# Kernel optimization log

Measured on AMD Instinct MI355X. Metric: run time of the kernel, lower is better.

## Reference

```python
import jax, jax.numpy as jnp
import numpy as np

B, S, V, D, H, NL, FF, MAXD, OUTLEN, NC = 8, 1024, 64, 512, 8, 6, 2048, 64, 8, 10
HD = D // H


def _layernorm(x, g, b, eps=1e-5):
    m = jnp.mean(x, axis=-1, keepdims=True)
    v = jnp.var(x, axis=-1, keepdims=True)
    return (x - m) * jax.lax.rsqrt(v + eps) * g + b


def setup_inputs() -> dict:
    key = jax.random.key(0)
    ks = jax.random.split(key, 24)
    s = 0.02
    inp = {
        'src': jax.random.randint(ks[0], (B, S), 0, V, dtype=jnp.int32),
        'src_pad_mask': jnp.zeros((B, S), dtype=bool),
        'embed': jax.random.normal(ks[1], (V, D), jnp.float32) * s,
        'cls_token': jnp.zeros((D,), jnp.float32),
        'qkv_w': jax.random.normal(ks[2], (NL, 3 * D, D), jnp.float32) * s,
        'qkv_b': jnp.zeros((NL, 3 * D), jnp.float32),
        'out_w': jax.random.normal(ks[3], (NL, D, D), jnp.float32) * s,
        'out_b': jnp.zeros((NL, D), jnp.float32),
        'rel_emb': jax.random.normal(ks[4], (NL, 2 * MAXD + 1, H), jnp.float32) * s,
        'ln1_g': jnp.ones((NL, D), jnp.float32),
        'ln1_b': jnp.zeros((NL, D), jnp.float32),
        'w1': jax.random.normal(ks[5], (NL, FF, D), jnp.float32) * s,
        'b1': jnp.zeros((NL, FF), jnp.float32),
        'w2': jax.random.normal(ks[6], (NL, D, FF), jnp.float32) * s,
        'b2': jnp.zeros((NL, D), jnp.float32),
        'ln2_g': jnp.ones((NL, D), jnp.float32),
        'ln2_b': jnp.zeros((NL, D), jnp.float32),
        'norm_g': jnp.ones((D,), jnp.float32),
        'norm_b': jnp.zeros((D,), jnp.float32),
        'cls_w': jax.random.normal(ks[7], (OUTLEN * NC, D), jnp.float32) * s,
        'cls_b': jnp.zeros((OUTLEN * NC,), jnp.float32),
    }
    return inp


def _forward(src, src_pad_mask, embed, cls_token, qkv_w, qkv_b, out_w, out_b,
             rel_emb, ln1_g, ln1_b, w1, b1, w2, b2, ln2_g, ln2_b,
             norm_g, norm_b, cls_w, cls_b):
    b = src.shape[0]
    x = embed[src]                                         # [B,S,D]
    cls = jnp.broadcast_to(cls_token, (b, 1, D))
    x = jnp.concatenate([cls, x], axis=1)                  # [B,L,D], L=S+1
    L = x.shape[1]
    full_mask = jnp.concatenate([jnp.zeros((b, 1), bool), src_pad_mask], axis=1)

    # relative position indices, shared across layers
    rel = jnp.arange(L)[None, :] - jnp.arange(L)[:, None]  # [L,L]
    maxd = (rel_emb.shape[1] - 1) // 2
    rel = jnp.clip(rel, -maxd, maxd) + maxd
    scale = HD ** -0.5
    neg = jnp.asarray(-1e9, x.dtype)

    def layer(x, p):
        (qw, qb, ow, ob, re, g1, be1, W1, B1, W2, B2, g2, be2) = p
        qkv = jnp.einsum('bld,ed->ble', x, qw) + qb        # [B,L,3D]
        q, k, v = jnp.split(qkv, 3, axis=-1)
        q = q.reshape(b, L, H, HD)
        k = k.reshape(b, L, H, HD)
        v = v.reshape(b, L, H, HD)
        scores = jnp.einsum('bqhd,bkhd->bhqk', q, k) * scale
        bias = re[rel]                                     # [L,L,H]
        scores = scores + jnp.transpose(bias, (2, 0, 1))[None]
        scores = jnp.where(full_mask[:, None, None, :], neg, scores)
        attn = jax.nn.softmax(scores, axis=-1)
        o = jnp.einsum('bhqk,bkhd->bqhd', attn, v).reshape(b, L, D)
        o = jnp.einsum('bld,ed->ble', o, ow) + ob
        x2 = _layernorm(x + o, g1, be1)
        h = jax.nn.gelu(jnp.einsum('bld,fd->blf', x2, W1) + B1, approximate=False)
        ff = jnp.einsum('blf,df->bld', h, W2) + B2
        x3 = _layernorm(x2 + ff, g2, be2)
        return x3, None

    xs = (qkv_w, qkv_b, out_w, out_b, rel_emb, ln1_g, ln1_b,
          w1, b1, w2, b2, ln2_g, ln2_b)
    x, _ = jax.lax.scan(layer, x, xs)
    x = _layernorm(x, norm_g, norm_b)
    cls_repr = x[:, 0, :]
    logits = jnp.einsum('bd,od->bo', cls_repr, cls_w) + cls_b
    return logits.reshape(b, OUTLEN, NC)


def reference(src, src_pad_mask, embed, cls_token, qkv_w, qkv_b, out_w, out_b,
              rel_emb, ln1_g, ln1_b, w1, b1, w2, b2, ln2_g, ln2_b,
              norm_g, norm_b, cls_w, cls_b):
    return _forward(src, src_pad_mask, embed, cls_token, qkv_w, qkv_b, out_w,
                    out_b, rel_emb, ln1_g, ln1_b, w1, b1, w2, b2, ln2_g,
                    ln2_b, norm_g, norm_b, cls_w, cls_b)
```

## Files before the change

### kernel.cpp

```cpp
#include <hip/hip_runtime.h>
#include <hip/hip_bf16.h>
#include <stdint.h>

#define B 8
#define S 1024
#define L 1025
#define D 512
#define H 8
#define HD 64
#define NL 6
#define FF 2048
#define MAXD 64
#define OUTLEN 8
#define NC 10

#define MP 8320

typedef __bf16 bf16;
typedef __bf16 bf16x8 __attribute__((ext_vector_type(8)));
typedef __bf16 bf16x4 __attribute__((ext_vector_type(4)));
typedef float f32x4 __attribute__((ext_vector_type(4)));

__device__ __forceinline__ float fexp2(float x) { return __builtin_amdgcn_exp2f(x); }

#define LGKM_BARRIER() asm volatile("s_waitcnt lgkmcnt(0)\ns_barrier" ::: "memory")

__device__ __forceinline__ void gld16(const void* g, void* l) {
    __builtin_amdgcn_global_load_lds(
        (const __attribute__((address_space(1))) unsigned int*)g,
        (__attribute__((address_space(3))) unsigned int*)l,
        16, 0, 0);
}

__device__ __forceinline__ float fast_gelu(float v) {
    float x = v * 0.70710678118654752f;
    float ax = fabsf(x);
    float t = 1.f / fmaf(0.3275911f, ax, 1.f);
    float poly = t * (0.254829592f + t * (-0.284496736f + t * (1.421413741f +
                 t * (-1.453152027f + t * 1.061405429f))));
    float e = fexp2(-ax * ax * 1.4426950408889634f);
    float erfv = 1.f - poly * e;
    erfv = copysignf(erfv, x);
    return 0.5f * v * (1.f + erfv);
}

__global__ __launch_bounds__(256) void cvt_k(const float* __restrict__ in,
                                             bf16* __restrict__ out, int n4)
{
    int i = blockIdx.x * 256 + threadIdx.x;
    if (i >= n4) return;
    float4 v = reinterpret_cast<const float4*>(in)[i];
    bf16x4 o;
    o[0] = (bf16)v.x; o[1] = (bf16)v.y; o[2] = (bf16)v.z; o[3] = (bf16)v.w;
    reinterpret_cast<bf16x4*>(out)[i] = o;
}

__global__ void embed_k(const int* __restrict__ src, const float* __restrict__ emb,
                        const float* __restrict__ cls, float* __restrict__ x,
                        bf16* __restrict__ xb)
{
    long i = (long)blockIdx.x * blockDim.x + threadIdx.x;
    if (i >= (long)B * L * D) return;
    int d = (int)(i % D);
    long bl = i / D;
    int l = (int)(bl % L);
    int b = (int)(bl / L);
    float v = (l == 0) ? cls[d] : emb[(long)src[b * S + (l - 1)] * D + d];
    x[i] = v;
    xb[i] = (bf16)v;
}

template<int ACT, int OBF, int BIAS, int RT>
__global__ __launch_bounds__(256) void mgemm(const bf16* __restrict__ A,
                                             const bf16* __restrict__ W,
                                             const float* __restrict__ bias,
                                             float* __restrict__ Cf,
                                             bf16* __restrict__ Cb,
                                             int N, int K, int LDA)
{
    __shared__ bf16 Asl[2][RT * 32];
    __shared__ bf16 Bsl[2][128 * 32];
    int tid = threadIdx.x;
    int m0 = blockIdx.y * RT;
    int n0 = blockIdx.x * 128;
    int lane = tid & 63;
    int w = tid >> 6;
    int wbase = tid & ~63;
    int kb = (lane >> 4) * 8;
    int rsel = lane & 15;
    constexpr int FJ = (RT == 128) ? 4 : 2;
    constexpr int CW = (RT == 128) ? 64 : 32;
    int wr, wc;
    if constexpr (RT == 128) { wr = w >> 1; wc = w & 1; }
    else                     { wr = 0;      wc = w;     }
    f32x4 acc[4][FJ] = {};

    auto stage = [&](int buf, int k0) {
        if constexpr (RT == 128) {
#pragma unroll
            for (int r = 0; r < 2; r++) {
                int s = r * 256 + tid;
                int sb = r * 256 + wbase;
                gld16(A + (size_t)(m0 + (s >> 2)) * LDA + k0 + (s & 3) * 8, &Asl[buf][(size_t)sb * 8]);
                gld16(W + (size_t)(n0 + (s >> 2)) * LDA + k0 + (s & 3) * 8, &Bsl[buf][(size_t)sb * 8]);
            }
        } else {
            gld16(A + (size_t)(m0 + (tid >> 2)) * LDA + k0 + (tid & 3) * 8, &Asl[buf][(size_t)wbase * 8]);
#pragma unroll
            for (int r = 0; r < 2; r++) {
                int s = r * 256 + tid;
                int sb = r * 256 + wbase;
                gld16(W + (size_t)(n0 + (s >> 2)) * LDA + k0 + (s & 3) * 8, &Bsl[buf][(size_t)sb * 8]);
            }
        }
    };

    stage(0, 0);
    __syncthreads();

    for (int k0 = 0; k0 < K; k0 += 32) {
        int cur = (k0 >> 5) & 1;
        if (k0 + 32 < K) stage(cur ^ 1, k0 + 32);
        bf16x8 af[4], bfr[FJ];
#pragma unroll
        for (int fi = 0; fi < 4; fi++)
            af[fi] = *reinterpret_cast<const bf16x8*>(&Asl[cur][(wr * 64 + fi * 16 + rsel) * 32 + kb]);
#pragma unroll
        for (int fj = 0; fj < FJ; fj++)
            bfr[fj] = *reinterpret_cast<const bf16x8*>(&Bsl[cur][(wc * CW + fj * 16 + rsel) * 32 + kb]);
#pragma unroll
        for (int fi = 0; fi < 4; fi++)
#pragma unroll
            for (int fj = 0; fj < FJ; fj++)
                acc[fi][fj] = __builtin_amdgcn_mfma_f32_16x16x32_bf16(af[fi], bfr[fj], acc[fi][fj], 0, 0, 0);
        __syncthreads();
    }
    int rowb = (lane >> 4) * 4;
    int colb = lane & 15;
#pragma unroll
    for (int fi = 0; fi < 4; fi++) {
#pragma unroll
        for (int fj = 0; fj < FJ; fj++) {
            int col = n0 + wc * CW + fj * 16 + colb;
            float bsv = BIAS ? bias[col] : 0.f;
#pragma unroll
            for (int i = 0; i < 4; i++) {
                int row = m0 + wr * 64 + fi * 16 + rowb + i;
                float v = acc[fi][fj][i] + bsv;
                if (ACT) v = fast_gelu(v);
                if (OBF) Cb[(size_t)row * N + col] = (bf16)v;
                else     Cf[(size_t)row * N + col] = v;
            }
        }
    }
}

__global__ __launch_bounds__(256) void fattn_k(const bf16* __restrict__ qkv,
                                               const float* __restrict__ rel_emb_l,
                                               const unsigned char* __restrict__ pad,
                                               bf16* __restrict__ ob)
{
    constexpr int PIT = 72;
    __shared__ bf16 Vt[3][64 * PIT];
    __shared__ bf16 Psh[4][2][16 * PIT];
    __shared__ float bias2s[2 * MAXD + 1];
    __shared__ float colm[2][64];

    const int bh = blockIdx.x;
    const int qt = blockIdx.y;
    const int h = bh & 7, b = bh >> 3;
    const int q0 = qt * 128;
    const int tid = threadIdx.x;
    const int lane = tid & 63;
    const int w = tid >> 6;
    const int ln15 = lane & 15, g4 = lane >> 4;
    const int kb8 = g4 * 8;
    constexpr float LOG2E = 1.4426950408889634f;
    constexpr float C2 = 0.125f * LOG2E;

    const char* base = (const char*)qkv + (size_t)(b * L) * 3072 + (size_t)h * (HD * 2);

    for (int i = tid; i < 2 * MAXD + 1; i += 256) bias2s[i] = rel_emb_l[i * H + h] * LOG2E;
    if (tid < 64) colm[0][tid] = (tid > 0 && pad[(size_t)b * S + tid - 1]) ? -1e9f : 0.f;

    int qrow[2];
    bf16x8 qa[2][2];
#pragma unroll
    for (int qq = 0; qq < 2; qq++) {
        qrow[qq] = q0 + qq * 64 + w * 16 + ln15;
        qa[qq][0] = *(const bf16x8*)(base + (size_t)qrow[qq] * 3072 + g4 * 16);
        qa[qq][1] = *(const bf16x8*)(base + (size_t)qrow[qq] * 3072 + 64 + g4 * 16);
    }

    const int vr = tid >> 3;
    const int vd0 = (tid & 7) * 8;
    const int vsw = ((vd0 >> 3) & 7) << 3;

    {
        bf16x8 a = *(const bf16x8*)(base + (size_t)vr * 3072 + 2048 + vd0 * 2);
        bf16x8 c = *(const bf16x8*)(base + (size_t)(vr + 32) * 3072 + 2048 + vd0 * 2);
#pragma unroll
        for (int j = 0; j < 8; j++) {
            Vt[0][(vd0 + j) * PIT + (vr ^ vsw)] = a[j];
            Vt[0][(vd0 + j) * PIT + ((vr + 32) ^ vsw)] = c[j];
        }
    }
    bf16x8 kr[4][2];
#pragma unroll
    for (int fj = 0; fj < 4; fj++) {
        const char* rp = base + (size_t)(fj * 16 + ln15) * 3072 + 1024 + g4 * 16;
        kr[fj][0] = *(const bf16x8*)(rp);
        kr[fj][1] = *(const bf16x8*)(rp + 64);
    }
    LGKM_BARRIER();

    f32x4 oacc[2][4] = {};
    float m_prev[2] = {-1e30f, -1e30f};
    float l_sum[2] = {0.f, 0.f};

    int cur3 = 0;
    for (int t = 0; t < 17; t++) {
        const int k0 = t * 64;
        const int k0n = (k0 + 64 > 1024) ? 1024 : (k0 + 64);
        const int curM = t & 1;
        int nxt3 = cur3 + 1; if (nxt3 == 3) nxt3 = 0;

        bf16x8 vA = *(const bf16x8*)(base + (size_t)(k0n + vr) * 3072 + 2048 + vd0 * 2);
        bf16x8 vB = *(const bf16x8*)(base + (size_t)(k0n + vr + 32) * 3072 + 2048 + vd0 * 2);

        f32x4 sacc[2][4] = {};
#pragma unroll
        for (int qq = 0; qq < 2; qq++)
#pragma unroll
            for (int fj = 0; fj < 4; fj++) {
                sacc[qq][fj] = __builtin_amdgcn_mfma_f32_16x16x32_bf16(kr[fj][0], qa[qq][0], sacc[qq][fj], 0, 0, 0);
                sacc[qq][fj] = __builtin_amdgcn_mfma_f32_16x16x32_bf16(kr[fj][1], qa[qq][1], sacc[qq][fj], 0, 0, 0);
            }
#pragma unroll
        for (int fj = 0; fj < 4; fj++) {
            const char* rp = base + (size_t)(k0n + fj * 16 + ln15) * 3072 + 1024 + g4 * 16;
            kr[fj][0] = *(const bf16x8*)(rp);
            kr[fj][1] = *(const bf16x8*)(rp + 64);
        }

        f32x4 cm[4];
#pragma unroll
        for (int fj = 0; fj < 4; fj++)
            cm[fj] = *(const f32x4*)&colm[curM][fj * 16 + g4 * 4];

#pragma unroll
        for (int qq = 0; qq < 2; qq++) {
            float sv[4][4];
            const int relbw = k0 - q0 - qq * 64 - w * 16;
            if (relbw >= MAXD + 15 || relbw <= -MAXD - 63) {
                const float bu = bias2s[relbw > 0 ? 2 * MAXD : 0];
#pragma unroll
                for (int fj = 0; fj < 4; fj++)
#pragma unroll
                    for (int i = 0; i < 4; i++)
                        sv[fj][i] = fmaf(sacc[qq][fj][i], C2, bu + cm[fj][i]);
            } else {
                const int relb = k0 - qrow[qq];
#pragma unroll
                for (int fj = 0; fj < 4; fj++)
#pragma unroll
                    for (int i = 0; i < 4; i++) {
                        int rel = relb + fj * 16 + g4 * 4 + i;
                        rel = rel < -MAXD ? -MAXD : (rel > MAXD ? MAXD : rel);
                        sv[fj][i] = fmaf(sacc[qq][fj][i], C2, bias2s[rel + MAXD] + cm[fj][i]);
                    }
            }

            float mx = sv[0][0];
#pragma unroll
            for (int fj = 0; fj < 4; fj++)
#pragma unroll
                for (int i = 0; i < 4; i++) mx = fmaxf(mx, sv[fj][i]);
            mx = fmaxf(mx, __shfl_xor(mx, 16));
            mx = fmaxf(mx, __shfl_xor(mx, 32));
            const float mnew = fmaxf(m_prev[qq], mx);
            const float corr = fexp2(m_prev[qq] - mnew);
            float rsum = 0.f;
            float pb[4][4];
#pragma unroll
            for (int fj = 0; fj < 4; fj++)
#pragma unroll
                for (int i = 0; i < 4; i++) {
                    float p = fexp2(sv[fj][i] - mnew);
                    pb[fj][i] = p;
                    rsum += p;
                }
            rsum += __shfl_xor(rsum, 16);
            rsum += __shfl_xor(rsum, 32);
            l_sum[qq] = l_sum[qq] * corr + rsum;
            m_prev[qq] = mnew;
#pragma unroll
            for (int fd = 0; fd < 4; fd++) oacc[qq][fd] *= corr;

#pragma unroll
            for (int fj = 0; fj < 4; fj++) {
                union { bf16 hh[4]; unsigned long long u; } pk;
                pk.hh[0] = (bf16)pb[fj][0]; pk.hh[1] = (bf16)pb[fj][1];
                pk.hh[2] = (bf16)pb[fj][2]; pk.hh[3] = (bf16)pb[fj][3];
                *(unsigned long long*)&Psh[w][qq][ln15 * PIT + fj * 16 + g4 * 4] = pk.u;
            }
        }

#pragma unroll
        for (int j = 0; j < 8; j++) {
            Vt[nxt3][(vd0 + j) * PIT + (vr ^ vsw)] = vA[j];
            Vt[nxt3][(vd0 + j) * PIT + ((vr + 32) ^ vsw)] = vB[j];
        }
        if (tid < 64) {
            int gk = k0 + 64 + tid;
            int pi = (gk <= 1024) ? gk - 1 : 0;
            colm[curM ^ 1][tid] = (gk > 1024 || pad[(size_t)b * S + pi]) ? -1e9f : 0.f;
        }

        LGKM_BARRIER();

        bf16x8 pa[2][2];
#pragma unroll
        for (int qq = 0; qq < 2; qq++) {
            pa[qq][0] = *(const bf16x8*)&Psh[w][qq][ln15 * PIT + kb8];
            pa[qq][1] = *(const bf16x8*)&Psh[w][qq][ln15 * PIT + 32 + kb8];
        }
#pragma unroll
        for (int fd = 0; fd < 4; fd++) {
            const int d = fd * 16 + ln15;
            const int vx = ((d >> 3) & 7) << 3;
            bf16x8 af0 = *(const bf16x8*)&Vt[cur3][d * PIT + (kb8 ^ vx)];
            bf16x8 af1 = *(const bf16x8*)&Vt[cur3][d * PIT + ((32 + kb8) ^ vx)];
            oacc[0][fd] = __builtin_amdgcn_mfma_f32_16x16x32_bf16(af0, pa[0][0], oacc[0][fd], 0, 0, 0);
            oacc[0][fd] = __builtin_amdgcn_mfma_f32_16x16x32_bf16(af1, pa[0][1], oacc[0][fd], 0, 0, 0);
            oacc[1][fd] = __builtin_amdgcn_mfma_f32_16x16x32_bf16(af0, pa[1][0], oacc[1][fd], 0, 0, 0);
            oacc[1][fd] = __builtin_amdgcn_mfma_f32_16x16x32_bf16(af1, pa[1][1], oacc[1][fd], 0, 0, 0);
        }
        cur3 = nxt3;
    }

#pragma unroll
    for (int qq = 0; qq < 2; qq++) {
        if (qrow[qq] < L) {
            const float inv = 1.f / l_sum[qq];
            bf16* op = ob + (size_t)(b * L + qrow[qq]) * D + h * HD + g4 * 4;
#pragma unroll
            for (int fd = 0; fd < 4; fd++) {
                bf16x4 r;
#pragma unroll
                for (int i = 0; i < 4; i++) r[i] = (bf16)(oacc[qq][fd][i] * inv);
                *(bf16x4*)(op + fd * 16) = r;
            }
        }
    }
}

__global__ __launch_bounds__(256) void add_ln_k(const float* __restrict__ xin,
                                                const float* __restrict__ rin,
                                                const float* __restrict__ g,
                                                const float* __restrict__ bb,
                                                float* __restrict__ out,
                                                bf16* __restrict__ outb)
{
    int row = blockIdx.x;
    __shared__ float red[8];
    int tid = threadIdx.x;
    const float* xp = xin + (size_t)row * D;
    const float* rp = rin + (size_t)row * D;
    float v0 = xp[tid] + rp[tid];
    float v1 = xp[tid + 256] + rp[tid + 256];
    float s = v0 + v1;
    for (int off = 32; off; off >>= 1) s += __shfl_down(s, off, 64);
    int lane = tid & 63, wid = tid >> 6;
    if (lane == 0) red[wid] = s;
    __syncthreads();
    if (tid == 0) red[0] = red[0] + red[1] + red[2] + red[3];
    __syncthreads();
    float mean = red[0] * (1.f / D);
    float d0 = v0 - mean, d1 = v1 - mean;
    float sq = d0 * d0 + d1 * d1;
    for (int off = 32; off; off >>= 1) sq += __shfl_down(sq, off, 64);
    if (lane == 0) red[4 + wid] = sq;
    __syncthreads();
    if (tid == 0) red[4] = red[4] + red[5] + red[6] + red[7];
    __syncthreads();
    float rs = rsqrtf(red[4] * (1.f / D) + 1e-5f);
    float r0 = d0 * rs * g[tid] + bb[tid];
    float r1 = d1 * rs * g[tid + 256] + bb[tid + 256];
    out[(size_t)row * D + tid] = r0;
    out[(size_t)row * D + tid + 256] = r1;
    outb[(size_t)row * D + tid] = (bf16)r0;
    outb[(size_t)row * D + tid + 256] = (bf16)r1;
}

__global__ __launch_bounds__(256) void cls_k(const float* __restrict__ x,
                                             const float* __restrict__ ng,
                                             const float* __restrict__ nb,
                                             const float* __restrict__ cw,
                                             const float* __restrict__ cb,
                                             float* __restrict__ out)
{
    int b = blockIdx.x;
    __shared__ float xn[D];
    __shared__ float red[8];
    int tid = threadIdx.x;
    const float* xp = x + (size_t)(b * L) * D;
    float v0 = xp[tid], v1 = xp[tid + 256];
    float s = v0 + v1;
    for (int off = 32; off; off >>= 1) s += __shfl_down(s, off, 64);
    int lane = tid & 63, wid = tid >> 6;
    if (lane == 0) red[wid] = s;
    __syncthreads();
    if (tid == 0) red[0] = red[0] + red[1] + red[2] + red[3];
    __syncthreads();
    float mean = red[0] * (1.f / D);
    float d0 = v0 - mean, d1 = v1 - mean;
    float sq = d0 * d0 + d1 * d1;
    for (int off = 32; off; off >>= 1) sq += __shfl_down(sq, off, 64);
    if (lane == 0) red[4 + wid] = sq;
    __syncthreads();
    if (tid == 0) red[4] = red[4] + red[5] + red[6] + red[7];
    __syncthreads();
    float rs = rsqrtf(red[4] * (1.f / D) + 1e-5f);
    xn[tid] = d0 * rs * ng[tid] + nb[tid];
    xn[tid + 256] = d1 * rs * ng[tid + 256] + nb[tid + 256];
    __syncthreads();
    for (int o = tid; o < OUTLEN * NC; o += 256) {
        float acc = cb[o];
        const float* wp = cw + (size_t)o * D;
        for (int d = 0; d < D; d++) acc += xn[d] * wp[d];
        out[b * OUTLEN * NC + o] = acc;
    }
}

extern "C" void kernel_launch(void* const* d_in, const int* in_sizes, int n_in,
                              void* d_out, int out_size, void* d_ws, size_t ws_size,
                              hipStream_t stream) {
    const int* src = (const int*)d_in[0];
    const unsigned char* pad = (const unsigned char*)d_in[1];
    const float* emb = (const float*)d_in[2];
    const float* cls_token = (const float*)d_in[3];
    const float* qkv_w = (const float*)d_in[4];
    const float* qkv_b = (const float*)d_in[5];
    const float* out_w = (const float*)d_in[6];
    const float* out_b = (const float*)d_in[7];
    const float* rel_emb = (const float*)d_in[8];
    const float* ln1_g = (const float*)d_in[9];
    const float* ln1_b = (const float*)d_in[10];
    const float* w1 = (const float*)d_in[11];
    const float* b1 = (const float*)d_in[12];
    const float* w2 = (const float*)d_in[13];
    const float* b2 = (const float*)d_in[14];
    const float* ln2_g = (const float*)d_in[15];
    const float* ln2_b = (const float*)d_in[16];
    const float* norm_g = (const float*)d_in[17];
    const float* norm_b = (const float*)d_in[18];
    const float* cls_w = (const float*)d_in[19];
    const float* cls_b = (const float*)d_in[20];
    float* out = (float*)d_out;

    char* ws = (char*)d_ws;
    size_t off = 0;
    float* x   = (float*)(ws + off); off += (size_t)MP * D * 4;
    bf16*  xb  = (bf16*) (ws + off); off += (size_t)MP * D * 2;
    float* x2  = (float*)(ws + off); off += (size_t)MP * D * 4;
    bf16*  x2b = (bf16*) (ws + off); off += (size_t)MP * D * 2;
    char*  R   = ws + off;           off += (size_t)MP * 3 * D * 4;
    bf16*  qkvb = (bf16*)R;
    bf16*  hb  = (bf16*)R;
    float* p   = (float*)(R + (size_t)MP * FF * 2);
    bf16*  obf = (bf16*) (ws + off); off += (size_t)MP * D * 2;

    const size_t WQ = (size_t)NL * 3 * D * D;
    const size_t WO = (size_t)NL * D * D;
    const size_t W1E = (size_t)NL * FF * D;
    const size_t W2E = (size_t)NL * D * FF;
    const size_t WALL = WQ + WO + W1E + W2E;
    bool all_w = (off + WALL * 2) <= ws_size;

    bf16 *wq_a = nullptr, *wo_a = nullptr, *w1_a = nullptr, *w2_a = nullptr, *wbuf = nullptr;
    if (all_w) {
        wq_a = (bf16*)(ws + off);
        wo_a = wq_a + WQ;
        w1_a = wo_a + WO;
        w2_a = w1_a + W1E;
        int n4;
        n4 = (int)(WQ / 4);  cvt_k<<<dim3((n4 + 255) / 256), 256, 0, stream>>>(qkv_w, wq_a, n4);
        n4 = (int)(WO / 4);  cvt_k<<<dim3((n4 + 255) / 256), 256, 0, stream>>>(out_w, wo_a, n4);
        n4 = (int)(W1E / 4); cvt_k<<<dim3((n4 + 255) / 256), 256, 0, stream>>>(w1, w1_a, n4);
        n4 = (int)(W2E / 4); cvt_k<<<dim3((n4 + 255) / 256), 256, 0, stream>>>(w2, w2_a, n4);
    } else {
        wbuf = (bf16*)(ws + off);
    }

    const int M = B * L;
    {
        long total = (long)B * L * D;
        embed_k<<<dim3((unsigned)((total + 255) / 256)), 256, 0, stream>>>(src, emb, cls_token, x, xb);
    }
    for (int l = 0; l < NL; l++) {
        const float* qb  = qkv_b + (size_t)l * 3 * D;
        const float* obi = out_b + (size_t)l * D;
        const float* re  = rel_emb + (size_t)l * (2 * MAXD + 1) * H;
        const float* g1  = ln1_g + (size_t)l * D;
        const float* be1 = ln1_b + (size_t)l * D;
        const float* B1p = b1 + (size_t)l * FF;
        const float* B2p = b2 + (size_t)l * D;
        const float* g2  = ln2_g + (size_t)l * D;
        const float* be2 = ln2_b + (size_t)l * D;

        const bf16 *wqb, *wob, *w1b, *w2b;
        if (all_w) {
            wqb = wq_a + (size_t)l * 3 * D * D;
            wob = wo_a + (size_t)l * D * D;
            w1b = w1_a + (size_t)l * FF * D;
            w2b = w2_a + (size_t)l * D * FF;
        } else {
            bf16* wp_ = wbuf;
            wqb = wp_;            wp_ += 3 * D * D;
            wob = wp_;            wp_ += D * D;
            w1b = wp_;            wp_ += FF * D;
            w2b = wp_;
            int n4;
            n4 = 3 * D * D / 4; cvt_k<<<dim3((n4 + 255) / 256), 256, 0, stream>>>(qkv_w + (size_t)l * 3 * D * D, (bf16*)wqb, n4);
            n4 = D * D / 4;     cvt_k<<<dim3((n4 + 255) / 256), 256, 0, stream>>>(out_w + (size_t)l * D * D, (bf16*)wob, n4);
            n4 = FF * D / 4;    cvt_k<<<dim3((n4 + 255) / 256), 256, 0, stream>>>(w1 + (size_t)l * FF * D, (bf16*)w1b, n4);
            n4 = D * FF / 4;    cvt_k<<<dim3((n4 + 255) / 256), 256, 0, stream>>>(w2 + (size_t)l * D * FF, (bf16*)w2b, n4);
        }

        mgemm<0, 1, 1, 128><<<dim3(3 * D / 128, MP / 128), 256, 0, stream>>>(xb, wqb, qb, nullptr, qkvb, 3 * D, D, D);
        fattn_k<<<dim3(B * H, 9), 256, 0, stream>>>(qkvb, re, pad, obf);
        mgemm<0, 0, 1, 64><<<dim3(D / 128, MP / 64), 256, 0, stream>>>(obf, wob, obi, p, nullptr, D, D, D);
        add_ln_k<<<dim3(M), 256, 0, stream>>>(x, p, g1, be1, x2, x2b);
        mgemm<1, 1, 1, 128><<<dim3(FF / 128, MP / 128), 256, 0, stream>>>(x2b, w1b, B1p, nullptr, hb, FF, D, D);
        mgemm<0, 0, 1, 64><<<dim3(D / 128, MP / 64), 256, 0, stream>>>(hb, w2b, B2p, p, nullptr, D, FF, FF);
        add_ln_k<<<dim3(M), 256, 0, stream>>>(x2, p, g2, be2, x, xb);
    }
    cls_k<<<dim3(B), 256, 0, stream>>>(x, norm_g, norm_b, cls_w, cls_b, out);
}
```

Measured before the change: 1.475 ms.

## Split attention over key range into two partials and merge with combine kernel

Adds a split-K (flash-decoding style) partition of the attention key loop: each block processes half of the key tiles and writes a partial normalized output plus per-row max and sum, then a new combine kernel merges the two halves using log-sum-exp rescaling. This doubles the grid from 576 blocks so more of the GPU's compute units are busy, since the original grid was small relative to the device. In exchange it adds an extra kernel launch, extra global traffic for partial outputs and stats, and an additional bf16 rounding of partial results. Scratch buffers x2b and p are reused for partials and stats.

New measurement: 1.463 ms. About the same (-0.8%).

```diff
diff --git a/kernel.cpp b/kernel.cpp
--- a/kernel.cpp
+++ b/kernel.cpp
@@ -158,7 +158,9 @@
 __global__ __launch_bounds__(256) void fattn_k(const bf16* __restrict__ qkv,
                                                const float* __restrict__ rel_emb_l,
                                                const unsigned char* __restrict__ pad,
-                                               bf16* __restrict__ ob)
+                                               bf16* __restrict__ op0,
+                                               bf16* __restrict__ op1,
+                                               float2* __restrict__ mlout)
 {
     constexpr int PIT = 72;
     __shared__ bf16 Vt[3][64 * PIT];
@@ -168,6 +170,10 @@
 
     const int bh = blockIdx.x;
     const int qt = blockIdx.y;
+    const int z = blockIdx.z;
+    const int tbeg = z ? 9 : 0;
+    const int tend = z ? 17 : 9;
+    bf16* opart = z ? op1 : op0;
     const int h = bh & 7, b = bh >> 3;
     const int q0 = qt * 128;
     const int tid = threadIdx.x;
@@ -181,7 +187,11 @@
     const char* base = (const char*)qkv + (size_t)(b * L) * 3072 + (size_t)h * (HD * 2);
 
     for (int i = tid; i < 2 * MAXD + 1; i += 256) bias2s[i] = rel_emb_l[i * H + h] * LOG2E;
-    if (tid < 64) colm[0][tid] = (tid > 0 && pad[(size_t)b * S + tid - 1]) ? -1e9f : 0.f;
+    if (tid < 64) {
+        int gk0 = tbeg * 64 + tid;
+        int pi = (gk0 > 0 && gk0 <= 1024) ? gk0 - 1 : 0;
+        colm[tbeg & 1][tid] = (gk0 > 1024 || (gk0 > 0 && pad[(size_t)b * S + pi])) ? -1e9f : 0.f;
+    }
 
     int qrow[2];
     bf16x8 qa[2][2];
@@ -197,8 +207,9 @@
     const int vsw = ((vd0 >> 3) & 7) << 3;
 
     {
-        bf16x8 a = *(const bf16x8*)(base + (size_t)vr * 3072 + 2048 + vd0 * 2);
-        bf16x8 c = *(const bf16x8*)(base + (size_t)(vr + 32) * 3072 + 2048 + vd0 * 2);
+        int kv0 = tbeg * 64;
+        bf16x8 a = *(const bf16x8*)(base + (size_t)(kv0 + vr) * 3072 + 2048 + vd0 * 2);
+        bf16x8 c = *(const bf16x8*)(base + (size_t)(kv0 + vr + 32) * 3072 + 2048 + vd0 * 2);
 #pragma unroll
         for (int j = 0; j < 8; j++) {
             Vt[0][(vd0 + j) * PIT + (vr ^ vsw)] = a[j];
@@ -208,7 +219,7 @@
     bf16x8 kr[4][2];
 #pragma unroll
     for (int fj = 0; fj < 4; fj++) {
-        const char* rp = base + (size_t)(fj * 16 + ln15) * 3072 + 1024 + g4 * 16;
+        const char* rp = base + (size_t)(tbeg * 64 + fj * 16 + ln15) * 3072 + 1024 + g4 * 16;
         kr[fj][0] = *(const bf16x8*)(rp);
         kr[fj][1] = *(const bf16x8*)(rp + 64);
     }
@@ -219,7 +230,7 @@
     float l_sum[2] = {0.f, 0.f};
 
     int cur3 = 0;
-    for (int t = 0; t < 17; t++) {
+    for (int t = tbeg; t < tend; t++) {
         const int k0 = t * 64;
         const int k0n = (k0 + 64 > 1024) ? 1024 : (k0 + 64);
         const int curM = t & 1;
@@ -343,7 +354,7 @@
     for (int qq = 0; qq < 2; qq++) {
         if (qrow[qq] < L) {
             const float inv = 1.f / l_sum[qq];
-            bf16* op = ob + (size_t)(b * L + qrow[qq]) * D + h * HD + g4 * 4;
+            bf16* op = opart + (size_t)(b * L + qrow[qq]) * D + h * HD + g4 * 4;
 #pragma unroll
             for (int fd = 0; fd < 4; fd++) {
                 bf16x4 r;
@@ -351,7 +362,35 @@
                 for (int i = 0; i < 4; i++) r[i] = (bf16)(oacc[qq][fd][i] * inv);
                 *(bf16x4*)(op + fd * 16) = r;
             }
-        }
+            if (g4 == 0)
+                mlout[(size_t)(z * 64 + b * 8 + h) * 1025 + qrow[qq]] =
+                    make_float2(m_prev[qq], l_sum[qq]);
+        }
+    }
+}
+
+__global__ __launch_bounds__(256) void comb_k(const bf16* __restrict__ op0,
+                                              const bf16* __restrict__ op1,
+                                              const float2* __restrict__ ml,
+                                              bf16* __restrict__ ob)
+{
+    int row = blockIdx.x;
+    int b = row / L, q = row - b * L;
+    int tid = threadIdx.x;
+    int d = tid & 63;
+    int h0 = tid >> 6;
+#pragma unroll
+    for (int hh = 0; hh < 2; hh++) {
+        int h = h0 + hh * 4;
+        float2 a = ml[(size_t)(b * 8 + h) * 1025 + q];
+        float2 c = ml[(size_t)(64 + b * 8 + h) * 1025 + q];
+        float m = fmaxf(a.x, c.x);
+        float s1 = a.y * fexp2(a.x - m);
+        float s2 = c.y * fexp2(c.x - m);
+        float inv = 1.f / (s1 + s2);
+        size_t idx = (size_t)row * D + h * HD + d;
+        float o = (s1 * (float)op0[idx] + s2 * (float)op1[idx]) * inv;
+        ob[idx] = (bf16)o;
     }
 }
 
@@ -471,6 +510,8 @@
     float* p   = (float*)(R + (size_t)MP * FF * 2);
     bf16*  obf = (bf16*) (ws + off); off += (size_t)MP * D * 2;
 
+    float2* mlbuf = (float2*)p;
+
     const size_t WQ = (size_t)NL * 3 * D * D;
     const size_t WO = (size_t)NL * D * D;
     const size_t W1E = (size_t)NL * FF * D;
@@ -529,7 +570,8 @@
         }
 
         mgemm<0, 1, 1, 128><<<dim3(3 * D / 128, MP / 128), 256, 0, stream>>>(xb, wqb, qb, nullptr, qkvb, 3 * D, D, D);
-        fattn_k<<<dim3(B * H, 9), 256, 0, stream>>>(qkvb, re, pad, obf);
+        fattn_k<<<dim3(B * H, 9, 2), 256, 0, stream>>>(qkvb, re, pad, x2b, obf, mlbuf);
+        comb_k<<<dim3(M), 256, 0, stream>>>(x2b, obf, mlbuf, obf);
         mgemm<0, 0, 1, 64><<<dim3(D / 128, MP / 64), 256, 0, stream>>>(obf, wob, obi, p, nullptr, D, D, D);
         add_ln_k<<<dim3(M), 256, 0, stream>>>(x, p, g1, be1, x2, x2b);
         mgemm<1, 1, 1, 128><<<dim3(FF / 128, MP / 128), 256, 0, stream>>>(x2b, w1b, B1p, nullptr, hb, FF, D, D);
```
